# Optimization experiments

Hardware: AMD Instinct MI355X
Metric: run time of the kernel (lower is better)

## Reference

```python
import jax, jax.numpy as jnp
import numpy as np

N = 32768          # total nodes
B = 64             # number of graphs (batch.max()+1)
IN_C = 256
OUT_C = 256
NUM_SCALES = 4
NUM_HEADS = 8
BN_EPS = 1e-5


def setup_inputs() -> dict:
    key = jax.random.key(0)
    ks = jax.random.split(key, 10)
    out_s = OUT_C // NUM_SCALES
    x = jax.random.normal(ks[0], (N, IN_C), jnp.float32)
    spectral = jax.random.normal(ks[1], (NUM_SCALES, N, IN_C), jnp.float32)
    batch = jnp.sort(jax.random.randint(ks[2], (N,), 0, B)).astype(jnp.int64)
    # per-scale Linear weights (glorot) and zero biases; stored as [S, in, out_s]
    g = (6.0 / (IN_C + out_s)) ** 0.5
    Ws = jax.random.uniform(ks[3], (NUM_SCALES, IN_C, out_s), jnp.float32, -g, g)
    bs = jnp.zeros((NUM_SCALES, out_s), jnp.float32)
    # MultiheadAttention params (torch layout: in_proj [3E,E], out_proj [E,E])
    s_in = (1.0 / OUT_C) ** 0.5
    W_in = jax.random.uniform(ks[4], (3 * OUT_C, OUT_C), jnp.float32, -s_in, s_in)
    b_in = jnp.zeros((3 * OUT_C,), jnp.float32)
    W_out = jax.random.uniform(ks[5], (OUT_C, OUT_C), jnp.float32, -s_in, s_in)
    b_out = jnp.zeros((OUT_C,), jnp.float32)
    gamma = jnp.ones((OUT_C,), jnp.float32)
    beta = jnp.zeros((OUT_C,), jnp.float32)
    return {"x": x, "spectral": spectral, "Ws": Ws, "bs": bs,
            "W_in": W_in, "b_in": b_in, "W_out": W_out, "b_out": b_out,
            "gamma": gamma, "beta": beta, "batch": batch}


def _forward(x, spectral, Ws, bs, W_in, b_in, W_out, b_out, gamma, beta, batch):
    n, E = x.shape[0], W_out.shape[0]
    # per-scale linear on (x + spectral_feat), concat over scales -> [N, E]
    scale_out = jnp.einsum('sni,sio->sno', x[None] + spectral, Ws) + bs[:, None, :]
    h = jnp.moveaxis(scale_out, 0, 1).reshape(n, E)
    # ragged -> dense padding (batch is sorted segment ids)
    counts = jnp.bincount(batch, length=B)
    max_nodes = int(np.asarray(counts).max())  # data-dependent pad, as in torch
    starts = jnp.concatenate([jnp.zeros((1,), counts.dtype), jnp.cumsum(counts)[:-1]])
    pos = jnp.arange(n) - starts[batch]
    h_pad = jnp.zeros((B, max_nodes, E), h.dtype).at[batch, pos].set(h)
    # MHA over padded graphs (no key-padding mask, matching the source)
    hd = E // NUM_HEADS
    qkv = h_pad @ W_in.T + b_in                       # [B, M, 3E]
    q, k, v = jnp.split(qkv, 3, axis=-1)
    def heads(t):
        return t.reshape(B, max_nodes, NUM_HEADS, hd).transpose(0, 2, 1, 3)
    q, k, v = heads(q) * (hd ** -0.5), heads(k), heads(v)
    attn = jax.nn.softmax(jnp.einsum('bhqd,bhkd->bhqk', q, k), axis=-1)
    ctx = jnp.einsum('bhqk,bhkd->bhqd', attn, v)
    ctx = ctx.transpose(0, 2, 1, 3).reshape(B, max_nodes, E)
    h_att = ctx @ W_out.T + b_out
    # dense -> ragged unpad
    h2 = h_att[batch, pos]                            # [N, E]
    # BatchNorm1d (training-mode batch stats, deterministic) + ReLU; dropout=eval
    mean = h2.mean(axis=0)
    var = h2.var(axis=0)
    hn = (h2 - mean) * jax.lax.rsqrt(var + BN_EPS) * gamma + beta
    return jax.nn.relu(hn)


def reference(x, spectral, Ws, bs, W_in, b_in, W_out, b_out, gamma, beta, batch):
    return _forward(x, spectral, Ws, bs, W_in, b_in, W_out, b_out, gamma, beta, batch)
```

## Files before the change

kernel.cpp:

```cpp
#include <hip/hip_runtime.h>


typedef __attribute__((ext_vector_type(8))) short frag8;
typedef __attribute__((ext_vector_type(4))) short frag4;
typedef __attribute__((ext_vector_type(4))) float f32x4;
typedef __attribute__((ext_vector_type(8))) unsigned short ushort8;
typedef __attribute__((ext_vector_type(2))) unsigned int uint2e;

#define NN 32768
#define NB 64
#define CIN 256
#define COUT 256
#define NHEAD 8
#define HD 32

#define BM 128
#define BK 64
#define LDK 72
#define KT 128

#if __has_builtin(__builtin_amdgcn_mfma_f32_16x16x16bf16_1k)
#define HAS_MFMA16 1
#else
#define HAS_MFMA16 0
#endif

__device__ inline unsigned short f2bf(float f) {
  unsigned u = __builtin_bit_cast(unsigned, f);
  u += 0x7FFFu + ((u >> 16) & 1u);
  return (unsigned short)(u >> 16);
}
__device__ inline float bf2f(unsigned short h) {
  return __builtin_bit_cast(float, (unsigned)h << 16);
}
__device__ inline unsigned pack2bf(float a, float b) {
  return (unsigned)f2bf(a) | ((unsigned)f2bf(b) << 16);
}

__global__ void k_prep(const float* __restrict__ Ws, const float* __restrict__ Win,
                       const float* __restrict__ Wout, const int* __restrict__ batch,
                       unsigned short* __restrict__ wst, unsigned short* __restrict__ winb,
                       unsigned short* __restrict__ woutb, int* __restrict__ meta) {
  int tid = blockIdx.x * 256 + threadIdx.x;
  if (tid < NN) {
    int v = batch[tid];
    int prev = (tid == 0) ? -1 : batch[tid - 1];
    for (int bb = prev + 1; bb <= v; ++bb) meta[NB + bb] = tid;
  }
  if (tid < 4 * 64 * 256) {
    int s = tid >> 14, rem = tid & 16383, o = rem >> 8, i = rem & 255;
    wst[tid] = f2bf(Ws[((s * 256) + i) * 64 + o]);
  } else if (tid < 4 * 64 * 256 + 768 * 256) {
    int t2 = tid - 4 * 64 * 256;
    winb[t2] = f2bf(Win[t2]);
  } else if (tid < 4 * 64 * 256 + 768 * 256 + 256 * 256) {
    int t3 = tid - (4 * 64 * 256 + 768 * 256);
    woutb[t3] = f2bf(Wout[t3]);
  }
}
__global__ void k_meta2(int* __restrict__ meta) {
  __shared__ int mx[NB];
  int b = threadIdx.x;
  int s = meta[NB + b];
  int e = (b == 63) ? NN : meta[NB + b + 1];
  meta[b] = e - s;
  mx[b] = e - s;
  __syncthreads();
  if (b == 0) {
    int m = 0;
    for (int j = 0; j < NB; ++j) m = max(m, mx[j]);
    meta[2 * NB] = m;
  }
}

template <int NT>
__device__ inline void mfma_tile(const unsigned short (*As)[LDK],
                                 const unsigned short (*Bs)[LDK],
                                 f32x4 acc[2][NT], int wave, int lane) {
  int m16 = lane & 15, quad = lane >> 4;
#pragma unroll
  for (int kk = 0; kk < 2; ++kk) {
    frag8 a[2], b[NT];
#pragma unroll
    for (int mi = 0; mi < 2; ++mi)
      a[mi] = *(const frag8*)&As[wave * 32 + mi * 16 + m16][kk * 32 + quad * 8];
#pragma unroll
    for (int ni = 0; ni < NT; ++ni)
      b[ni] = *(const frag8*)&Bs[ni * 16 + m16][kk * 32 + quad * 8];
#pragma unroll
    for (int mi = 0; mi < 2; ++mi)
#pragma unroll
      for (int ni = 0; ni < NT; ++ni)
        acc[mi][ni] = __builtin_amdgcn_mfma_f32_16x16x32_bf16(a[mi], b[ni], acc[mi][ni], 0, 0, 0);
  }
}

__device__ inline void stage_B64(const unsigned short* __restrict__ Wt, int c0, int k0,
                                 unsigned short (*Bs)[LDK], int t) {
  int n = t & 63, seg = t >> 6;
  const unsigned short* src = Wt + (size_t)(c0 + n) * 256 + k0 + seg * 16;
  uint4 v0 = *(const uint4*)src;
  uint4 v1 = *(const uint4*)(src + 8);
  *(uint4*)&Bs[n][seg * 16] = v0;
  *(uint4*)&Bs[n][seg * 16 + 8] = v1;
}

__device__ inline void stage_B128(const unsigned short* __restrict__ Wt, int c0, int k0,
                                  unsigned short (*Bs)[LDK], int t) {
  int n = t >> 1, half = t & 1;
  const unsigned short* src = Wt + (size_t)(c0 + n) * 256 + k0 + half * 32;
#pragma unroll
  for (int i = 0; i < 4; ++i) {
    uint4 v = *(const uint4*)(src + i * 8);
    *(uint4*)&Bs[n][half * 32 + i * 8] = v;
  }
}

__device__ inline void stage_A_bf(const unsigned short* __restrict__ A, int lda, int r0, int k0,
                                  unsigned short (*As)[LDK], int t) {
  int r = t >> 1, half = t & 1;
  const unsigned short* src = A + (size_t)(r0 + r) * lda + k0 + half * 32;
#pragma unroll
  for (int i = 0; i < 4; ++i) {
    uint4 v = *(const uint4*)(src + i * 8);
    *(uint4*)&As[r][half * 32 + i * 8] = v;
  }
}

__global__ __launch_bounds__(256) void k_scale(const float* __restrict__ x,
                                               const float* __restrict__ spec,
                                               const unsigned short* __restrict__ wst,
                                               const float* __restrict__ bs,
                                               unsigned short* __restrict__ h) {
  __shared__ unsigned short As[BM][LDK];
  __shared__ unsigned short Bs[64][LDK];
  int t = threadIdx.x, lane = t & 63, wave = t >> 6;
  int r0 = blockIdx.x * BM, s = blockIdx.y;
  f32x4 z = {0.f, 0.f, 0.f, 0.f};
  f32x4 acc[2][4];
#pragma unroll
  for (int mi = 0; mi < 2; ++mi)
#pragma unroll
    for (int ni = 0; ni < 4; ++ni) acc[mi][ni] = z;

  const float* sb = spec + (size_t)s * NN * CIN;
  for (int k0 = 0; k0 < CIN; k0 += BK) {
    {
      int r = t >> 1, half = t & 1;
      const float* xs = x + (size_t)(r0 + r) * CIN + k0 + half * 32;
      const float* ss = sb + (size_t)(r0 + r) * CIN + k0 + half * 32;
#pragma unroll
      for (int i = 0; i < 8; ++i) {
        float4 xv = *(const float4*)(xs + i * 4);
        float4 sv = *(const float4*)(ss + i * 4);
        ushort4 o;
        o.x = f2bf(xv.x + sv.x); o.y = f2bf(xv.y + sv.y);
        o.z = f2bf(xv.z + sv.z); o.w = f2bf(xv.w + sv.w);
        *(ushort4*)&As[r][half * 32 + i * 4] = o;
      }
    }
    stage_B64(wst + (size_t)s * 64 * 256, 0, k0, Bs, t);
    __syncthreads();
    mfma_tile<4>(As, Bs, acc, wave, lane);
    __syncthreads();
  }
  int m16 = lane & 15, quad = lane >> 4;
#pragma unroll
  for (int mi = 0; mi < 2; ++mi)
#pragma unroll
    for (int ni = 0; ni < 4; ++ni) {
      int col = ni * 16 + m16;
      float bias = bs[s * 64 + col];
#pragma unroll
      for (int r = 0; r < 4; ++r) {
        int row = r0 + wave * 32 + mi * 16 + quad * 4 + r;
        h[(size_t)row * COUT + s * 64 + col] = f2bf(acc[mi][ni][r] + bias);
      }
    }
}

template <int LDOUT, bool F32OUT, bool STATS>
__global__ __launch_bounds__(256) void k_lin(const unsigned short* __restrict__ A,
                                             const unsigned short* __restrict__ Wt,
                                             const float* __restrict__ bias,
                                             void* __restrict__ out,
                                             float* __restrict__ sums) {
  __shared__ unsigned short As[BM][LDK];
  __shared__ unsigned short Bs[128][LDK];
  int t = threadIdx.x, lane = t & 63, wave = t >> 6;
  int r0 = blockIdx.x * BM, c0 = blockIdx.y * 128;
  f32x4 z = {0.f, 0.f, 0.f, 0.f};
  f32x4 acc[2][8];
#pragma unroll
  for (int mi = 0; mi < 2; ++mi)
#pragma unroll
    for (int ni = 0; ni < 8; ++ni) acc[mi][ni] = z;

  for (int k0 = 0; k0 < 256; k0 += BK) {
    stage_A_bf(A, 256, r0, k0, As, t);
    stage_B128(Wt, c0, k0, Bs, t);
    __syncthreads();
    mfma_tile<8>(As, Bs, acc, wave, lane);
    __syncthreads();
  }
  int m16 = lane & 15, quad = lane >> 4;
  float cs[8], cs2[8];
#pragma unroll
  for (int ni = 0; ni < 8; ++ni) { cs[ni] = 0.f; cs2[ni] = 0.f; }
#pragma unroll
  for (int mi = 0; mi < 2; ++mi)
#pragma unroll
    for (int ni = 0; ni < 8; ++ni) {
      int col = c0 + ni * 16 + m16;
      float bv = bias[col];
#pragma unroll
      for (int r = 0; r < 4; ++r) {
        int row = r0 + wave * 32 + mi * 16 + quad * 4 + r;
        float v = acc[mi][ni][r] + bv;
        if constexpr (STATS) { cs[ni] += v; cs2[ni] += v * v; }
        if constexpr (F32OUT)
          ((float*)out)[(size_t)row * LDOUT + col] = v;
        else
          ((unsigned short*)out)[(size_t)row * LDOUT + col] = f2bf(v);
      }
    }
  if constexpr (STATS) {
#pragma unroll
    for (int ni = 0; ni < 8; ++ni) {
      float a = cs[ni], b2 = cs2[ni];
      a += __shfl_xor(a, 16); a += __shfl_xor(a, 32);
      b2 += __shfl_xor(b2, 16); b2 += __shfl_xor(b2, 32);
      if (quad == 0) {
        atomicAdd(&sums[c0 + ni * 16 + m16], a);
        atomicAdd(&sums[256 + c0 + ni * 16 + m16], b2);
      }
    }
  }
}

__global__ __launch_bounds__(256) void k_attn_mfma(const unsigned short* __restrict__ qkv,
                                                   const int* __restrict__ meta,
                                                   unsigned short* __restrict__ ctx) {
  int b = blockIdx.x >> 3, head = blockIdx.x & 7;
  int c = meta[b], st = meta[NB + b], M = meta[2 * NB];
  int q0 = blockIdx.y * 128;
  if (q0 >= c) return;

  __shared__ unsigned short Vt[32][KT + 8];

  int t = threadIdx.x, lane = t & 63, wave = t >> 6;
  int m16 = lane & 15, quad = lane >> 4;
  const float SCALE = 0.17677669529663687f;
  float extra = (float)(M - c);

  int qbase = q0 + wave * 32;
  frag8 qf[2];
#pragma unroll
  for (int qg = 0; qg < 2; ++qg) {
    int qrow = qbase + qg * 16 + m16;
    qf[qg] = *(const frag8*)(qkv + (size_t)(st + qrow) * 768 + head * 32 + quad * 8);
  }

  f32x4 zz = {0.f, 0.f, 0.f, 0.f};
  f32x4 O[2][2];
  float lp[2] = {0.f, 0.f};
#pragma unroll
  for (int qg = 0; qg < 2; ++qg) { O[qg][0] = zz; O[qg][1] = zz; }

#if !HAS_MFMA16
  int sl0 = m16 + ((quad & 1) << 5);
  int sl1 = sl0 + 16;
#endif

  for (int kt = 0; kt < c; kt += KT) {
    {
      int key = t >> 1, dh0 = (t & 1) * 16;
      const unsigned short* vp = qkv + (size_t)(st + kt + key) * 768 + 512 + head * 32 + dh0;
      ushort8 v0 = *(const ushort8*)vp;
      ushort8 v1 = *(const ushort8*)(vp + 8);
#pragma unroll
      for (int i = 0; i < 8; ++i) {
        Vt[dh0 + i][key] = v0[i];
        Vt[dh0 + 8 + i][key] = v1[i];
      }
    }
    __syncthreads();

#pragma unroll
    for (int sub = 0; sub < 4; ++sub) {
      int ks = kt + sub * 32;
      if (ks < c) {
        bool full = (ks + 32 <= c);
        frag8 kf[2];
#pragma unroll
        for (int kh = 0; kh < 2; ++kh) {
          int krow = ks + kh * 16 + m16;
          kf[kh] = *(const frag8*)(qkv + (size_t)(st + krow) * 768 + 256 + head * 32 + quad * 8);
        }
        unsigned pk[2][2][2];
#pragma unroll
        for (int qg = 0; qg < 2; ++qg)
#pragma unroll
          for (int kh = 0; kh < 2; ++kh) {
            f32x4 s = __builtin_amdgcn_mfma_f32_16x16x32_bf16(kf[kh], qf[qg], zz, 0, 0, 0);
            float p[4];
#pragma unroll
            for (int r = 0; r < 4; ++r) p[r] = __expf(s[r] * SCALE);
            if (!full) {
#pragma unroll
              for (int r = 0; r < 4; ++r)
                if (ks + kh * 16 + quad * 4 + r >= c) p[r] = 0.f;
            }
            lp[qg] += (p[0] + p[1]) + (p[2] + p[3]);
            pk[qg][kh][0] = pack2bf(p[0], p[1]);
            pk[qg][kh][1] = pack2bf(p[2], p[3]);
          }
#if HAS_MFMA16
        frag4 vb[2][2];
#pragma unroll
        for (int kh = 0; kh < 2; ++kh)
#pragma unroll
          for (int dh = 0; dh < 2; ++dh)
            vb[kh][dh] = *(const frag4*)&Vt[dh * 16 + m16][sub * 32 + kh * 16 + quad * 4];
#pragma unroll
        for (int qg = 0; qg < 2; ++qg) {
          frag4 pa0 = __builtin_bit_cast(frag4, uint2e{pk[qg][0][0], pk[qg][0][1]});
          frag4 pa1 = __builtin_bit_cast(frag4, uint2e{pk[qg][1][0], pk[qg][1][1]});
#pragma unroll
          for (int dh = 0; dh < 2; ++dh) {
            O[qg][dh] = __builtin_amdgcn_mfma_f32_16x16x16bf16_1k(pa0, vb[0][dh], O[qg][dh], 0, 0, 0);
            O[qg][dh] = __builtin_amdgcn_mfma_f32_16x16x16bf16_1k(pa1, vb[1][dh], O[qg][dh], 0, 0, 0);
          }
        }
#else
        frag8 vf[2];
#pragma unroll
        for (int dh = 0; dh < 2; ++dh)
          vf[dh] = *(const frag8*)&Vt[dh * 16 + m16][sub * 32 + quad * 8];
#pragma unroll
        for (int qg = 0; qg < 2; ++qg) {
          unsigned a0 = __shfl(pk[qg][0][0], sl0), a1 = __shfl(pk[qg][0][1], sl0);
          unsigned a2 = __shfl(pk[qg][0][0], sl1), a3 = __shfl(pk[qg][0][1], sl1);
          unsigned b0 = __shfl(pk[qg][1][0], sl0), b1 = __shfl(pk[qg][1][1], sl0);
          unsigned b2 = __shfl(pk[qg][1][0], sl1), b3 = __shfl(pk[qg][1][1], sl1);
          uint4 pw;
          pw.x = (quad < 2) ? a0 : b0;
          pw.y = (quad < 2) ? a1 : b1;
          pw.z = (quad < 2) ? a2 : b2;
          pw.w = (quad < 2) ? a3 : b3;
          frag8 pf = __builtin_bit_cast(frag8, pw);
#pragma unroll
          for (int dh = 0; dh < 2; ++dh)
            O[qg][dh] = __builtin_amdgcn_mfma_f32_16x16x32_bf16(pf, vf[dh], O[qg][dh], 0, 0, 0);
        }
#endif
      }
    }
    __syncthreads();
  }

#pragma unroll
  for (int qg = 0; qg < 2; ++qg) {
    float v = lp[qg];
    v += __shfl_xor(v, 16);
    v += __shfl_xor(v, 32);
    lp[qg] = v;
  }

#pragma unroll
  for (int qg = 0; qg < 2; ++qg)
#pragma unroll
    for (int r = 0; r < 4; ++r) {
      int qrow = qbase + qg * 16 + quad * 4 + r;
      float lsum = __shfl(lp[qg], quad * 4 + r);
      if (qrow < c) {
        float inv = 1.f / (lsum + extra);
        unsigned short* op = ctx + (size_t)(st + qrow) * 256 + head * 32;
        op[m16] = f2bf(O[qg][0][r] * inv);
        op[16 + m16] = f2bf(O[qg][1][r] * inv);
      }
    }
}

__global__ __launch_bounds__(256) void k_bn_apply(const unsigned short* __restrict__ h,
                                                  const float* __restrict__ sums,
                                                  const float* __restrict__ gamma,
                                                  const float* __restrict__ beta,
                                                  float* __restrict__ out) {
  size_t i8 = ((size_t)blockIdx.x * 256 + threadIdx.x) * 8;
  int c0 = (int)(i8 & 255);
  ushort8 v = *(const ushort8*)(h + i8);
  float4 o0, o1;
  float res[8];
#pragma unroll
  for (int i = 0; i < 8; ++i) {
    int ch = c0 + i;
    float mean = sums[ch] * (1.0f / NN);
    float var = sums[256 + ch] * (1.0f / NN) - mean * mean;
    float sc = rsqrtf(var + 1e-5f) * gamma[ch];
    float sh = beta[ch] - mean * sc;
    res[i] = fmaxf(bf2f(v[i]) * sc + sh, 0.f);
  }
  o0.x = res[0]; o0.y = res[1]; o0.z = res[2]; o0.w = res[3];
  o1.x = res[4]; o1.y = res[5]; o1.z = res[6]; o1.w = res[7];
  *(float4*)(out + i8) = o0;
  *(float4*)(out + i8 + 4) = o1;
}

extern "C" void kernel_launch(void* const* d_in, const int* in_sizes, int n_in,
                              void* d_out, int out_size, void* d_ws, size_t ws_size,
                              hipStream_t stream) {
  const float* x      = (const float*)d_in[0];
  const float* spec   = (const float*)d_in[1];
  const float* Ws     = (const float*)d_in[2];
  const float* bs     = (const float*)d_in[3];
  const float* Win    = (const float*)d_in[4];
  const float* b_in   = (const float*)d_in[5];
  const float* Wout   = (const float*)d_in[6];
  const float* b_out  = (const float*)d_in[7];
  const float* gamma  = (const float*)d_in[8];
  const float* beta   = (const float*)d_in[9];
  const int* batch    = (const int*)d_in[10];
  float* out = (float*)d_out;

  char* w = (char*)d_ws;
  size_t off = 0;
  auto alloc = [&](size_t bytes) -> void* {
    off = (off + 255) & ~(size_t)255;
    void* p = w + off; off += bytes; return p;
  };
  int* meta             = (int*)alloc(129 * sizeof(int));
  unsigned short* wst   = (unsigned short*)alloc((size_t)4 * 64 * 256 * 2);
  unsigned short* winb  = (unsigned short*)alloc((size_t)768 * 256 * 2);
  unsigned short* woutb = (unsigned short*)alloc((size_t)256 * 256 * 2);
  float* sums           = (float*)alloc(512 * 4);
  unsigned short* h     = (unsigned short*)alloc((size_t)NN * 256 * 2);
  unsigned short* qkv   = (unsigned short*)alloc((size_t)NN * 768 * 2);
  unsigned short* ctx   = (unsigned short*)alloc((size_t)NN * 256 * 2);
  unsigned short* hatt  = (unsigned short*)alloc((size_t)NN * 256 * 2);

  (void)hipMemsetAsync(sums, 0, 512 * 4, stream);
  k_prep<<<1280, 256, 0, stream>>>(Ws, Win, Wout, batch, wst, winb, woutb, meta);
  k_meta2<<<1, 64, 0, stream>>>(meta);
  k_scale<<<dim3(NN / BM, 4), 256, 0, stream>>>(x, spec, wst, bs, h);
  k_lin<768, false, false><<<dim3(NN / BM, 6), 256, 0, stream>>>(h, winb, b_in, qkv, nullptr);
  k_attn_mfma<<<dim3(NB * NHEAD, 8), 256, 0, stream>>>(qkv, meta, ctx);
  k_lin<256, false, true><<<dim3(NN / BM, 2), 256, 0, stream>>>(ctx, woutb, b_out, hatt, sums);
  k_bn_apply<<<NN * 256 / 2048, 256, 0, stream>>>(hatt, sums, gamma, beta, out);
}
```

Measured before the change: 416.2 us.

## Stage full weight panel in LDS and load A fragments directly from global

The GEMM kernels (scale projection, QKV and output projection) now load the whole 64-column weight panel into shared memory once. They read A operands straight from global memory into MFMA fragments, which removes the per-K-step A staging and barriers. The linear kernels use narrower 64-column tiles with twice the grid width. BatchNorm statistics move out of the output-projection epilogue into a separate k_stats kernel. This trades A-tile reuse across waves in LDS for fewer syncs, at the cost of more global traffic for A and an extra pass over hatt.

```diff
diff --git a/kernel.cpp b/kernel.cpp
--- a/kernel.cpp
+++ b/kernel.cpp
@@ -15,8 +15,7 @@
 #define HD 32
 
 #define BM 128
-#define BK 64
-#define LDK 72
+#define LDB 264
 #define KT 128
 
 #if __has_builtin(__builtin_amdgcn_mfma_f32_16x16x16bf16_1k)
@@ -73,69 +72,31 @@
   }
 }
 
-template <int NT>
-__device__ inline void mfma_tile(const unsigned short (*As)[LDK],
-                                 const unsigned short (*Bs)[LDK],
-                                 f32x4 acc[2][NT], int wave, int lane) {
-  int m16 = lane & 15, quad = lane >> 4;
-#pragma unroll
-  for (int kk = 0; kk < 2; ++kk) {
-    frag8 a[2], b[NT];
-#pragma unroll
-    for (int mi = 0; mi < 2; ++mi)
-      a[mi] = *(const frag8*)&As[wave * 32 + mi * 16 + m16][kk * 32 + quad * 8];
-#pragma unroll
-    for (int ni = 0; ni < NT; ++ni)
-      b[ni] = *(const frag8*)&Bs[ni * 16 + m16][kk * 32 + quad * 8];
-#pragma unroll
-    for (int mi = 0; mi < 2; ++mi)
-#pragma unroll
-      for (int ni = 0; ni < NT; ++ni)
-        acc[mi][ni] = __builtin_amdgcn_mfma_f32_16x16x32_bf16(a[mi], b[ni], acc[mi][ni], 0, 0, 0);
-  }
-}
-
-__device__ inline void stage_B64(const unsigned short* __restrict__ Wt, int c0, int k0,
-                                 unsigned short (*Bs)[LDK], int t) {
-  int n = t & 63, seg = t >> 6;
-  const unsigned short* src = Wt + (size_t)(c0 + n) * 256 + k0 + seg * 16;
-  uint4 v0 = *(const uint4*)src;
-  uint4 v1 = *(const uint4*)(src + 8);
-  *(uint4*)&Bs[n][seg * 16] = v0;
-  *(uint4*)&Bs[n][seg * 16 + 8] = v1;
-}
-
-__device__ inline void stage_B128(const unsigned short* __restrict__ Wt, int c0, int k0,
-                                  unsigned short (*Bs)[LDK], int t) {
-  int n = t >> 1, half = t & 1;
-  const unsigned short* src = Wt + (size_t)(c0 + n) * 256 + k0 + half * 32;
-#pragma unroll
-  for (int i = 0; i < 4; ++i) {
+__device__ inline void stage_Bpanel(const unsigned short* __restrict__ Wt,
+                                    unsigned short (*Bs)[LDB], int t) {
+  int n = t >> 2, seg = t & 3;
+  const unsigned short* src = Wt + (size_t)n * 256 + seg * 64;
+#pragma unroll
+  for (int i = 0; i < 8; ++i) {
     uint4 v = *(const uint4*)(src + i * 8);
-    *(uint4*)&Bs[n][half * 32 + i * 8] = v;
-  }
-}
-
-__device__ inline void stage_A_bf(const unsigned short* __restrict__ A, int lda, int r0, int k0,
-                                  unsigned short (*As)[LDK], int t) {
-  int r = t >> 1, half = t & 1;
-  const unsigned short* src = A + (size_t)(r0 + r) * lda + k0 + half * 32;
-#pragma unroll
-  for (int i = 0; i < 4; ++i) {
-    uint4 v = *(const uint4*)(src + i * 8);
-    *(uint4*)&As[r][half * 32 + i * 8] = v;
-  }
-}
+    *(uint4*)&Bs[n][seg * 64 + i * 8] = v;
+  }
+}
+
 
 __global__ __launch_bounds__(256) void k_scale(const float* __restrict__ x,
                                                const float* __restrict__ spec,
                                                const unsigned short* __restrict__ wst,
                                                const float* __restrict__ bs,
                                                unsigned short* __restrict__ h) {
-  __shared__ unsigned short As[BM][LDK];
-  __shared__ unsigned short Bs[64][LDK];
+  __shared__ unsigned short Bs[64][LDB];
   int t = threadIdx.x, lane = t & 63, wave = t >> 6;
   int r0 = blockIdx.x * BM, s = blockIdx.y;
+  int m16 = lane & 15, quad = lane >> 4;
+
+  stage_Bpanel(wst + (size_t)s * 64 * 256, Bs, t);
+  __syncthreads();
+
   f32x4 z = {0.f, 0.f, 0.f, 0.f};
   f32x4 acc[2][4];
 #pragma unroll
@@ -144,27 +105,35 @@
     for (int ni = 0; ni < 4; ++ni) acc[mi][ni] = z;
 
   const float* sb = spec + (size_t)s * NN * CIN;
-  for (int k0 = 0; k0 < CIN; k0 += BK) {
-    {
-      int r = t >> 1, half = t & 1;
-      const float* xs = x + (size_t)(r0 + r) * CIN + k0 + half * 32;
-      const float* ss = sb + (size_t)(r0 + r) * CIN + k0 + half * 32;
-#pragma unroll
-      for (int i = 0; i < 8; ++i) {
-        float4 xv = *(const float4*)(xs + i * 4);
-        float4 sv = *(const float4*)(ss + i * 4);
-        ushort4 o;
-        o.x = f2bf(xv.x + sv.x); o.y = f2bf(xv.y + sv.y);
-        o.z = f2bf(xv.z + sv.z); o.w = f2bf(xv.w + sv.w);
-        *(ushort4*)&As[r][half * 32 + i * 4] = o;
-      }
-    }
-    stage_B64(wst + (size_t)s * 64 * 256, 0, k0, Bs, t);
-    __syncthreads();
-    mfma_tile<4>(As, Bs, acc, wave, lane);
-    __syncthreads();
-  }
-  int m16 = lane & 15, quad = lane >> 4;
+#pragma unroll
+  for (int kc = 0; kc < 8; ++kc) {
+    int kb = kc * 32 + quad * 8;
+    frag8 a[2];
+#pragma unroll
+    for (int mi = 0; mi < 2; ++mi) {
+      size_t base = (size_t)(r0 + wave * 32 + mi * 16 + m16) * CIN + kb;
+      float4 x0 = *(const float4*)(x + base);
+      float4 x1 = *(const float4*)(x + base + 4);
+      float4 s0 = *(const float4*)(sb + base);
+      float4 s1 = *(const float4*)(sb + base + 4);
+      uint4 u;
+      u.x = pack2bf(x0.x + s0.x, x0.y + s0.y);
+      u.y = pack2bf(x0.z + s0.z, x0.w + s0.w);
+      u.z = pack2bf(x1.x + s1.x, x1.y + s1.y);
+      u.w = pack2bf(x1.z + s1.z, x1.w + s1.w);
+      a[mi] = __builtin_bit_cast(frag8, u);
+    }
+    frag8 b[4];
+#pragma unroll
+    for (int ni = 0; ni < 4; ++ni)
+      b[ni] = *(const frag8*)&Bs[ni * 16 + m16][kc * 32 + quad * 8];
+#pragma unroll
+    for (int mi = 0; mi < 2; ++mi)
+#pragma unroll
+      for (int ni = 0; ni < 4; ++ni)
+        acc[mi][ni] = __builtin_amdgcn_mfma_f32_16x16x32_bf16(a[mi], b[ni], acc[mi][ni], 0, 0, 0);
+  }
+
 #pragma unroll
   for (int mi = 0; mi < 2; ++mi)
 #pragma unroll
@@ -179,63 +148,56 @@
     }
 }
 
-template <int LDOUT, bool F32OUT, bool STATS>
+template <int LDOUT>
 __global__ __launch_bounds__(256) void k_lin(const unsigned short* __restrict__ A,
                                              const unsigned short* __restrict__ Wt,
                                              const float* __restrict__ bias,
-                                             void* __restrict__ out,
-                                             float* __restrict__ sums) {
-  __shared__ unsigned short As[BM][LDK];
-  __shared__ unsigned short Bs[128][LDK];
+                                             unsigned short* __restrict__ out) {
+  __shared__ unsigned short Bs[64][LDB];
   int t = threadIdx.x, lane = t & 63, wave = t >> 6;
-  int r0 = blockIdx.x * BM, c0 = blockIdx.y * 128;
+  int r0 = blockIdx.x * BM, c0 = blockIdx.y * 64;
+  int m16 = lane & 15, quad = lane >> 4;
+
+  stage_Bpanel(Wt + (size_t)c0 * 256, Bs, t);
+  __syncthreads();
+
   f32x4 z = {0.f, 0.f, 0.f, 0.f};
-  f32x4 acc[2][8];
+  f32x4 acc[2][4];
 #pragma unroll
   for (int mi = 0; mi < 2; ++mi)
 #pragma unroll
-    for (int ni = 0; ni < 8; ++ni) acc[mi][ni] = z;
-
-  for (int k0 = 0; k0 < 256; k0 += BK) {
-    stage_A_bf(A, 256, r0, k0, As, t);
-    stage_B128(Wt, c0, k0, Bs, t);
-    __syncthreads();
-    mfma_tile<8>(As, Bs, acc, wave, lane);
-    __syncthreads();
-  }
-  int m16 = lane & 15, quad = lane >> 4;
-  float cs[8], cs2[8];
-#pragma unroll
-  for (int ni = 0; ni < 8; ++ni) { cs[ni] = 0.f; cs2[ni] = 0.f; }
+    for (int ni = 0; ni < 4; ++ni) acc[mi][ni] = z;
+
+#pragma unroll
+  for (int kc = 0; kc < 8; ++kc) {
+    int kb = kc * 32 + quad * 8;
+    frag8 a[2];
+#pragma unroll
+    for (int mi = 0; mi < 2; ++mi)
+      a[mi] = *(const frag8*)(A + (size_t)(r0 + wave * 32 + mi * 16 + m16) * 256 + kb);
+    frag8 b[4];
+#pragma unroll
+    for (int ni = 0; ni < 4; ++ni)
+      b[ni] = *(const frag8*)&Bs[ni * 16 + m16][kc * 32 + quad * 8];
+#pragma unroll
+    for (int mi = 0; mi < 2; ++mi)
+#pragma unroll
+      for (int ni = 0; ni < 4; ++ni)
+        acc[mi][ni] = __builtin_amdgcn_mfma_f32_16x16x32_bf16(a[mi], b[ni], acc[mi][ni], 0, 0, 0);
+  }
+
 #pragma unroll
   for (int mi = 0; mi < 2; ++mi)
 #pragma unroll
-    for (int ni = 0; ni < 8; ++ni) {
+    for (int ni = 0; ni < 4; ++ni) {
       int col = c0 + ni * 16 + m16;
       float bv = bias[col];
 #pragma unroll
       for (int r = 0; r < 4; ++r) {
         int row = r0 + wave * 32 + mi * 16 + quad * 4 + r;
-        float v = acc[mi][ni][r] + bv;
-        if constexpr (STATS) { cs[ni] += v; cs2[ni] += v * v; }
-        if constexpr (F32OUT)
-          ((float*)out)[(size_t)row * LDOUT + col] = v;
-        else
-          ((unsigned short*)out)[(size_t)row * LDOUT + col] = f2bf(v);
+        out[(size_t)row * LDOUT + col] = f2bf(acc[mi][ni][r] + bv);
       }
     }
-  if constexpr (STATS) {
-#pragma unroll
-    for (int ni = 0; ni < 8; ++ni) {
-      float a = cs[ni], b2 = cs2[ni];
-      a += __shfl_xor(a, 16); a += __shfl_xor(a, 32);
-      b2 += __shfl_xor(b2, 16); b2 += __shfl_xor(b2, 32);
-      if (quad == 0) {
-        atomicAdd(&sums[c0 + ni * 16 + m16], a);
-        atomicAdd(&sums[256 + c0 + ni * 16 + m16], b2);
-      }
-    }
-  }
 }
 
 __global__ __launch_bounds__(256) void k_attn_mfma(const unsigned short* __restrict__ qkv,
@@ -380,6 +342,20 @@
         op[16 + m16] = f2bf(O[qg][1][r] * inv);
       }
     }
+}
+
+__global__ __launch_bounds__(256) void k_stats(const unsigned short* __restrict__ h,
+                                               float* __restrict__ sums) {
+  int c = threadIdx.x;
+  int r0 = blockIdx.x * 64;
+  float s = 0.f, s2 = 0.f;
+#pragma unroll 8
+  for (int r = 0; r < 64; ++r) {
+    float v = bf2f(h[(size_t)(r0 + r) * 256 + c]);
+    s += v; s2 += v * v;
+  }
+  atomicAdd(&sums[c], s);
+  atomicAdd(&sums[256 + c], s2);
 }
 
 __global__ __launch_bounds__(256) void k_bn_apply(const unsigned short* __restrict__ h,
@@ -443,8 +419,9 @@
   k_prep<<<1280, 256, 0, stream>>>(Ws, Win, Wout, batch, wst, winb, woutb, meta);
   k_meta2<<<1, 64, 0, stream>>>(meta);
   k_scale<<<dim3(NN / BM, 4), 256, 0, stream>>>(x, spec, wst, bs, h);
-  k_lin<768, false, false><<<dim3(NN / BM, 6), 256, 0, stream>>>(h, winb, b_in, qkv, nullptr);
+  k_lin<768><<<dim3(NN / BM, 12), 256, 0, stream>>>(h, winb, b_in, qkv);
   k_attn_mfma<<<dim3(NB * NHEAD, 8), 256, 0, stream>>>(qkv, meta, ctx);
-  k_lin<256, false, true><<<dim3(NN / BM, 2), 256, 0, stream>>>(ctx, woutb, b_out, hatt, sums);
+  k_lin<256><<<dim3(NN / BM, 4), 256, 0, stream>>>(ctx, woutb, b_out, hatt);
+  k_stats<<<NN / 64, 256, 0, stream>>>(hatt, sums);
   k_bn_apply<<<NN * 256 / 2048, 256, 0, stream>>>(hatt, sums, gamma, beta, out);
 }
```

Measured after the change: 410.7 us. About the same (-1.3%).
